# Performance work log

Measured on AMD Instinct MI355X. Metric: run time of the kernel, lower is better.

## Reference

```python
import jax, jax.numpy as jnp
import numpy as np

MI, DIS, DIN, HID, L, H, NG, H1, OUT = 2048, 1024, 3072, 256, 15, 8, 8, 512, 64
DENOM = 4.0 / 7.0  # (grid_max - grid_min) / (num_grids - 1)
EPS = 1e-5


def _ln(x, g, b):
    m = jnp.mean(x, axis=-1, keepdims=True)
    v = jnp.mean((x - m) ** 2, axis=-1, keepdims=True)
    return (x - m) * jax.lax.rsqrt(v + EPS) * g + b


def _fastkan(x, ln_g, ln_b, grid, Ws, Wb, bb):
    xn = _ln(x, ln_g, ln_b)
    basis = jnp.exp(-(((xn[..., None] - grid) / DENOM) ** 2))  # [N, DIN, NG]
    ret = basis.reshape(x.shape[0], -1) @ Ws.T                  # SplineLinear (no bias)
    return ret + jax.nn.silu(x) @ Wb.T + bb                      # base update


def _hgcn(x, G, W, attn, bias, rW1, rb1, rW2, rb2, ln_g, ln_b, jk_W, jk_b):
    # per-layer multi-head conv: mean_h a_h * G @ (x @ W_h) == G @ (x @ (sum_h a_h W_h / H))
    def step(xc, p):
        W_l, a_l, b_l, rW1_l, rb1_l, rW2_l, rb2_l, g_l, be_l = p
        W_eff = jnp.einsum('h,hio->io', a_l, W_l) / H
        out = G @ (xc @ W_eff) + b_l
        gate = jax.nn.sigmoid(jax.nn.relu(out @ rW1_l.T + rb1_l) @ rW2_l.T + rb2_l)
        out = _ln(out * gate, g_l, be_l)
        out = jnp.where(out >= 0, out, 0.25 * out)  # leaky_relu(0.25); dropout off (eval)
        return out, out
    _, outs = jax.lax.scan(step, x, (W, attn, bias, rW1, rb1, rW2, rb2, ln_g, ln_b))
    jk = jnp.moveaxis(outs, 0, 1).reshape(x.shape[0], L * HID)   # jumping-knowledge concat
    return jk @ jk_W.T + jk_b


def _mlp3(x, W1, b1, W2, b2, W3, b3):
    h = jax.nn.relu(x @ W1.T + b1)
    h = jax.nn.relu(h @ W2.T + b2)
    return jax.nn.relu(h @ W3.T + b3)


def _forward(concat_mi, concat_dis, G_mi, G_dis, AT, A, rbf_grid, mi_kan_ln_g, mi_kan_ln_b, mi_kan_Ws, mi_kan_Wb, mi_kan_bb, dis_kan_ln_g, dis_kan_ln_b, dis_kan_Ws, dis_kan_Wb, dis_kan_bb, mi_W, mi_attn, mi_bias, mi_rW1, mi_rb1, mi_rW2, mi_rb2, mi_ln_g, mi_ln_b, mi_jk_W, mi_jk_b, dis_W, dis_attn, dis_bias, dis_rW1, dis_rb1, dis_rW2, dis_rb2, dis_ln_g, dis_ln_b, dis_jk_W, dis_jk_b, lx_W1, lx_b1, lx_W2, lx_b2, lx_W3, lx_b3, ly_W1, ly_b1, ly_W2, ly_b2, ly_W3, ly_b3, ne_W, ne_b, he_W, he_b, mun_W, mun_b, mue_W, mue_b):
    # AT and A are accepted by the original forward but never used in its body.
    mi_e = _fastkan(concat_mi, mi_kan_ln_g, mi_kan_ln_b, rbf_grid, mi_kan_Ws, mi_kan_Wb, mi_kan_bb)
    dis_e = _fastkan(concat_dis, dis_kan_ln_g, dis_kan_ln_b, rbf_grid, dis_kan_Ws, dis_kan_Wb, dis_kan_bb)
    mi_f = _hgcn(mi_e, G_mi, mi_W, mi_attn, mi_bias, mi_rW1, mi_rb1, mi_rW2, mi_rb2, mi_ln_g, mi_ln_b, mi_jk_W, mi_jk_b)
    dis_f = _hgcn(dis_e, G_dis, dis_W, dis_attn, dis_bias, dis_rW1, dis_rb1, dis_rW2, dis_rb2, dis_ln_g, dis_ln_b, dis_jk_W, dis_jk_b)
    x = _mlp3(mi_f, lx_W1, lx_b1, lx_W2, lx_b2, lx_W3, lx_b3)
    y = _mlp3(dis_f, ly_W1, ly_b1, ly_W2, ly_b2, ly_W3, ly_b3)
    result_h = x @ y.T                                           # [MI, DIS]
    z_node = jax.nn.relu(concat_mi @ ne_W.T + ne_b)              # node_encoders1 (eval: no dropout)
    z_edge = jax.nn.relu(concat_dis @ he_W.T + he_b)             # hyperedge_encoders1
    z_node_mean = z_node @ mun_W.T + mun_b                       # _enc_mu_node (identity act)
    z_edge_mean = z_edge @ mue_W.T + mue_b                       # _enc_mu_hedge
    recon = z_node_mean @ z_edge_mean.T                          # decoder2 with identity act
    score = 0.7 * jax.nn.sigmoid(recon) + 0.3 * jax.nn.sigmoid(result_h)
    return score, recon


def setup_inputs() -> dict:
    ks = iter(jax.random.split(jax.random.key(0), 96))
    nrm = lambda shape, s: jax.random.normal(next(ks), shape, dtype=jnp.float32) * s
    uni = lambda shape: jax.random.uniform(next(ks), shape, dtype=jnp.float32)
    d = {}
    d['concat_mi'] = nrm((MI, DIN), 1.0)
    d['concat_dis'] = nrm((DIS, DIN), 1.0)
    d['G_mi'] = uni((MI, MI)) / MI    # row-normalized dense hypergraph adjacency
    d['G_dis'] = uni((DIS, DIS)) / DIS
    d['AT'] = uni((DIS, MI))
    d['A'] = uni((MI, DIS))
    d['rbf_grid'] = jnp.linspace(-2.0, 2.0, NG).astype(jnp.float32)
    for p in ('mi', 'dis'):
        d[p + '_kan_ln_g'] = jnp.ones((DIN,), jnp.float32)
        d[p + '_kan_ln_b'] = jnp.zeros((DIN,), jnp.float32)
        d[p + '_kan_Ws'] = nrm((HID, DIN * NG), 0.02)
        d[p + '_kan_Wb'] = nrm((HID, DIN), 0.02)
        d[p + '_kan_bb'] = nrm((HID,), 0.01)
        d[p + '_W'] = nrm((L, H, HID, HID), 0.06)
        d[p + '_attn'] = jnp.ones((L, H), jnp.float32)
        d[p + '_bias'] = nrm((L, HID), 0.01)
        d[p + '_rW1'] = nrm((L, HID // 4, HID), 0.05)
        d[p + '_rb1'] = nrm((L, HID // 4), 0.01)
        d[p + '_rW2'] = nrm((L, HID, HID // 4), 0.05)
        d[p + '_rb2'] = nrm((L, HID), 0.01)
        d[p + '_ln_g'] = jnp.ones((L, HID), jnp.float32)
        d[p + '_ln_b'] = jnp.zeros((L, HID), jnp.float32)
        d[p + '_jk_W'] = nrm((HID, L * HID), 0.02)
        d[p + '_jk_b'] = nrm((HID,), 0.01)
    for p in ('lx', 'ly'):
        d[p + '_W1'] = nrm((256, HID), 0.05); d[p + '_b1'] = nrm((256,), 0.01)
        d[p + '_W2'] = nrm((128, 256), 0.05); d[p + '_b2'] = nrm((128,), 0.01)
        d[p + '_W3'] = nrm((64, 128), 0.05); d[p + '_b3'] = nrm((64,), 0.01)
    d['ne_W'] = nrm((H1, DIN), 0.02); d['ne_b'] = nrm((H1,), 0.01)
    d['he_W'] = nrm((H1, DIN), 0.02); d['he_b'] = nrm((H1,), 0.01)
    d['mun_W'] = nrm((OUT, H1), 0.02); d['mun_b'] = nrm((OUT,), 0.01)
    d['mue_W'] = nrm((OUT, H1), 0.02); d['mue_b'] = nrm((OUT,), 0.01)
    return d


def reference(concat_mi, concat_dis, G_mi, G_dis, AT, A, rbf_grid, mi_kan_ln_g, mi_kan_ln_b, mi_kan_Ws, mi_kan_Wb, mi_kan_bb, dis_kan_ln_g, dis_kan_ln_b, dis_kan_Ws, dis_kan_Wb, dis_kan_bb, mi_W, mi_attn, mi_bias, mi_rW1, mi_rb1, mi_rW2, mi_rb2, mi_ln_g, mi_ln_b, mi_jk_W, mi_jk_b, dis_W, dis_attn, dis_bias, dis_rW1, dis_rb1, dis_rW2, dis_rb2, dis_ln_g, dis_ln_b, dis_jk_W, dis_jk_b, lx_W1, lx_b1, lx_W2, lx_b2, lx_W3, lx_b3, ly_W1, ly_b1, ly_W2, ly_b2, ly_W3, ly_b3, ne_W, ne_b, he_W, he_b, mun_W, mun_b, mue_W, mue_b):
    return _forward(concat_mi, concat_dis, G_mi, G_dis, AT, A, rbf_grid, mi_kan_ln_g, mi_kan_ln_b, mi_kan_Ws, mi_kan_Wb, mi_kan_bb, dis_kan_ln_g, dis_kan_ln_b, dis_kan_Ws, dis_kan_Wb, dis_kan_bb, mi_W, mi_attn, mi_bias, mi_rW1, mi_rb1, mi_rW2, mi_rb2, mi_ln_g, mi_ln_b, mi_jk_W, mi_jk_b, dis_W, dis_attn, dis_bias, dis_rW1, dis_rb1, dis_rW2, dis_rb2, dis_ln_g, dis_ln_b, dis_jk_W, dis_jk_b, lx_W1, lx_b1, lx_W2, lx_b2, lx_W3, lx_b3, ly_W1, ly_b1, ly_W2, ly_b2, ly_W3, ly_b3, ne_W, ne_b, he_W, he_b, mun_W, mun_b, mue_W, mue_b)
```

## Files before the change

kernel.cpp:

```cpp
#include <hip/hip_runtime.h>
#include <cstdint>
#include <cstddef>

typedef unsigned short u16;
typedef __attribute__((ext_vector_type(8))) short short8;
typedef __attribute__((ext_vector_type(4))) float f32x4;

#define MI_N  2048
#define DIS_N 1024
#define TOT_N 3072
#define DIN   3072
#define HID   256
#define LL    15
#define NG    8

__device__ __forceinline__ float b2f(u16 u) {
  unsigned int v = ((unsigned int)u) << 16;
  float f;
  __builtin_memcpy(&f, &v, 4);
  return f;
}
__device__ __forceinline__ u16 f2b(float f) {
  unsigned int u;
  __builtin_memcpy(&u, &f, 4);
  u = (u + 0x7fffu + ((u >> 16) & 1u)) >> 16;
  return (u16)u;
}
__device__ __forceinline__ float sigf(float x) { return 1.f / (1.f + __expf(-x)); }
__device__ __forceinline__ unsigned cvtpk(float a, float b) {
  unsigned r;
  asm("v_cvt_pk_bf16_f32 %0, %1, %2" : "=v"(r) : "v"(a), "v"(b));
  return r;
}

#define NSEG 20
struct CvtJobs {
  const float* src[NSEG];
  u16* dst[NSEG];
  int nblk[NSEG];
  int nseg;
};

__global__ __launch_bounds__(256) void cvt_f2b(CvtJobs j) {
  int b = blockIdx.x, s = 0;
  while (s + 1 < j.nseg && b >= j.nblk[s]) { b -= j.nblk[s]; ++s; }
  const long base = ((long)b * 256 + threadIdx.x) * 8;
  const float4 v0 = *(const float4*)(j.src[s] + base);
  const float4 v1 = *(const float4*)(j.src[s] + base + 4);
  short8 o;
  o[0] = (short)f2b(v0.x); o[1] = (short)f2b(v0.y);
  o[2] = (short)f2b(v0.z); o[3] = (short)f2b(v0.w);
  o[4] = (short)f2b(v1.x); o[5] = (short)f2b(v1.y);
  o[6] = (short)f2b(v1.z); o[7] = (short)f2b(v1.w);
  *(short8*)(j.dst[s] + base) = o;
}

struct GP {
  const u16* A; int lda;
  const u16* B; int ldb;
  void* C; int ldc;
  const float* bias;
  int K;
  int mblk;
};

template <int ACT, int TRANS, int F32OUT, int NCT>
__global__ __launch_bounds__(256) void gemm_bt(GP p0, GP p1) {
  GP p = p0;
  int bx = blockIdx.x;
  if (bx >= p0.mblk) { bx -= p0.mblk; p = p1; }
  const int tid = threadIdx.x;
  const int w = tid >> 6;
  const int lane = tid & 63;
  const int m16 = lane & 15, quad = lane >> 4;
  const int kph = quad * 8;
  const long row0 = (long)bx * 32 + m16;
  const long colBase = (long)blockIdx.y * (16 * NCT);
  f32x4 acc[2][NCT] = {};
  const u16* A0 = p.A + row0 * (long)p.lda + kph;
  const u16* A1 = A0 + 16L * p.lda;
  const u16* Bb = p.B + (colBase + m16) * (long)p.ldb + kph;
  const long bstep = 16L * p.ldb;
  for (int kk = w * 32; kk < p.K; kk += 128) {
    short8 a0 = *(const short8*)(A0 + kk);
    short8 a1 = *(const short8*)(A1 + kk);
#pragma unroll
    for (int c = 0; c < NCT; ++c) {
      short8 b = *(const short8*)(Bb + c * bstep + kk);
      acc[0][c] = __builtin_amdgcn_mfma_f32_16x16x32_bf16(a0, b, acc[0][c], 0, 0, 0);
      acc[1][c] = __builtin_amdgcn_mfma_f32_16x16x32_bf16(a1, b, acc[1][c], 0, 0, 0);
    }
  }
  __shared__ float red[2][64][NCT * 8 + 1];
  float* av = (float*)acc;
  if (w >= 2) {
#pragma unroll
    for (int i = 0; i < NCT * 8; ++i) red[w - 2][lane][i] = av[i];
  }
  __syncthreads();
  if (w < 2) {
#pragma unroll
    for (int i = 0; i < NCT * 8; ++i) av[i] += red[w][lane][i];
  }
  __syncthreads();
  if (w == 1) {
#pragma unroll
    for (int i = 0; i < NCT * 8; ++i) red[0][lane][i] = av[i];
  }
  __syncthreads();
  if (w != 0) return;
#pragma unroll
  for (int i = 0; i < NCT * 8; ++i) av[i] += red[0][lane][i];
#pragma unroll
  for (int c = 0; c < NCT; ++c) {
    const long col = colBase + c * 16 + m16;
    const float bv = p.bias ? p.bias[col] : 0.f;
#pragma unroll
    for (int r = 0; r < 2; ++r) {
      const long orow = (long)bx * 32 + r * 16 + quad * 4;
#pragma unroll
      for (int j = 0; j < 4; ++j) {
        float v = acc[r][c][j] + bv;
        if (ACT == 1) v = fmaxf(v, 0.f);
        if (ACT == 2) v = sigf(v);
        if (F32OUT)
          ((float*)p.C)[(orow + j) * (long)p.ldc + col] = v;
        else if (TRANS)
          ((u16*)p.C)[col * (long)p.ldc + orow + j] = f2b(v);
        else
          ((u16*)p.C)[(orow + j) * (long)p.ldc + col] = f2b(v);
      }
    }
  }
}

struct FKP {
  const u16* xn; const u16* xb;
  const u16* Ws; const u16* Wb;
  float* partial;
  int rowoff;
  int mblk;
};

__global__ __launch_bounds__(256) void fastkan_gemm(FKP p0, FKP p1, const float* grid8) {
  FKP p = p0;
  int bx = blockIdx.x;
  if (bx >= p0.mblk) { bx -= p0.mblk; p = p1; }
  const int chunk = blockIdx.z;
  const int tid = threadIdx.x;
  const int w = tid >> 6;
  const int lane = tid & 63;
  const int m16 = lane & 15, quad = lane >> 4, kph = quad * 8;
  const long row0 = (long)bx * 16 + m16;
  f32x4 acc[16] = {};
  if (chunk < 8) {
    float gv[8];
#pragma unroll
    for (int j = 0; j < 8; ++j) gv[j] = grid8[j];
    const u16* xn0 = p.xn + row0 * (long)DIN;
    const int d0 = chunk * 384 + w * 4 + quad;
    u16 xr[24];
#pragma unroll
    for (int t = 0; t < 24; ++t) xr[t] = xn0[d0 + 16 * t];
    const u16* Bb = p.Ws + (long)m16 * (DIN * NG) + chunk * 3072 + w * 32 + kph;
#pragma unroll 2
    for (int t = 0; t < 24; ++t) {
      const float x0 = b2f(xr[t]);
      union { short8 s; unsigned u[4]; } a0;
#pragma unroll
      for (int jj = 0; jj < 4; ++jj) {
        float da = x0 - gv[2 * jj];
        float db = x0 - gv[2 * jj + 1];
        a0.u[jj] = cvtpk(__expf(da * da * -3.0625f), __expf(db * db * -3.0625f));
      }
#pragma unroll
      for (int c = 0; c < 16; ++c) {
        short8 b = *(const short8*)(Bb + (long)c * (16 * DIN * NG) + t * 128);
        acc[c] = __builtin_amdgcn_mfma_f32_16x16x32_bf16(a0.s, b, acc[c], 0, 0, 0);
      }
    }
  } else {
    const u16* x0p = p.xb + row0 * (long)DIN + kph;
    const u16* Bb = p.Wb + (long)m16 * DIN + w * 32 + kph;
#pragma unroll 2
    for (int t = 0; t < 24; ++t) {
      const int kk = w * 32 + t * 128;
      short8 r0 = *(const short8*)(x0p + kk);
      union { short8 s; unsigned u[4]; } a0;
#pragma unroll
      for (int jj = 0; jj < 4; ++jj) {
        float va = b2f((u16)r0[2 * jj]);
        float vb = b2f((u16)r0[2 * jj + 1]);
        a0.u[jj] = cvtpk(va * sigf(va), vb * sigf(vb));
      }
#pragma unroll
      for (int c = 0; c < 16; ++c) {
        short8 b = *(const short8*)(Bb + (long)c * (16 * DIN) + t * 128);
        acc[c] = __builtin_amdgcn_mfma_f32_16x16x32_bf16(a0.s, b, acc[c], 0, 0, 0);
      }
    }
  }
  __shared__ float red[2][64][65];
  float* av = (float*)acc;
  if (w >= 2) {
#pragma unroll
    for (int i = 0; i < 64; ++i) red[w - 2][lane][i] = av[i];
  }
  __syncthreads();
  if (w < 2) {
#pragma unroll
    for (int i = 0; i < 64; ++i) av[i] += red[w][lane][i];
  }
  __syncthreads();
  if (w == 1) {
#pragma unroll
    for (int i = 0; i < 64; ++i) red[0][lane][i] = av[i];
  }
  __syncthreads();
  if (w != 0) return;
#pragma unroll
  for (int i = 0; i < 64; ++i) av[i] += red[0][lane][i];
  float* outp = p.partial + ((long)chunk * TOT_N + p.rowoff) * HID;
#pragma unroll
  for (int c = 0; c < 16; ++c) {
    const long col = c * 16 + m16;
    const long orow = (long)bx * 16 + quad * 4;
#pragma unroll
    for (int j = 0; j < 4; ++j) outp[(orow + j) * HID + col] = acc[c][j];
  }
}

__global__ __launch_bounds__(256) void fk_combine(const float* partial, const float* bb_mi,
                                                  const float* bb_dis, u16* e) {
  const long i = (long)blockIdx.x * 256 + threadIdx.x;
  const int c = (int)(i & 255);
  const long n = i >> 8;
  float s = 0.f;
#pragma unroll
  for (int pI = 0; pI < 9; ++pI) s += partial[(long)pI * TOT_N * HID + i];
  s += (n < MI_N ? bb_mi : bb_dis)[c];
  e[i] = f2b(s);
}

__global__ __launch_bounds__(256) void weff_kernel(const float* Wmi, const float* Ami,
                                                   const float* Wdis, const float* Adis,
                                                   u16* outT) {
  const int b = blockIdx.x;
  const int s = b / 3840;
  const int r = b % 3840;
  const int l = r >> 8;
  const int t = r & 255;
  const int i0 = (t >> 4) << 4;
  const int o0 = (t & 15) << 4;
  const float* W = (s ? Wdis : Wmi) + (long)l * 8 * 65536;
  const float* A = (s ? Adis : Ami) + l * 8;
  const int tx = threadIdx.x & 15;
  const int ty = threadIdx.x >> 4;
  float sum = 0.f;
#pragma unroll
  for (int h = 0; h < 8; ++h)
    sum += A[h] * W[(long)h * 65536 + (long)(i0 + ty) * 256 + o0 + tx];
  sum *= 0.125f;
  __shared__ float tile[16][17];
  tile[ty][tx] = sum;
  __syncthreads();
  outT[((long)s * LL + l) * 65536 + (long)(o0 + ty) * 256 + i0 + tx] = f2b(tile[tx][ty]);
}

__device__ __forceinline__ void breduce2(float& a, float& b) {
  for (int o = 32; o > 0; o >>= 1) {
    a += __shfl_down(a, o);
    b += __shfl_down(b, o);
  }
  __shared__ float sm[8];
  const int w = threadIdx.x >> 6;
  const int lane = threadIdx.x & 63;
  if (lane == 0) { sm[w] = a; sm[4 + w] = b; }
  __syncthreads();
  if (threadIdx.x == 0) {
    sm[0] = sm[0] + sm[1] + sm[2] + sm[3];
    sm[4] = sm[4] + sm[5] + sm[6] + sm[7];
  }
  __syncthreads();
  a = sm[0];
  b = sm[4];
}

__global__ __launch_bounds__(256) void ln_silu(const float* xmi, const float* xdis,
                                               const float* gmi, const float* bmi,
                                               const float* gdis, const float* bdis,
                                               u16* xn, u16* cbf) {
  const int n = blockIdx.x;
  const bool ds = (n >= MI_N);
  const float* x = ds ? xdis + (long)(n - MI_N) * DIN : xmi + (long)n * DIN;
  const float* g = ds ? gdis : gmi;
  const float* be = ds ? bdis : bmi;
  float xv[12];
  float s1 = 0.f, s2 = 0.f;
#pragma unroll
  for (int j = 0; j < 12; ++j) {
    xv[j] = x[j * 256 + threadIdx.x];
    s1 += xv[j];
    s2 += xv[j] * xv[j];
  }
  breduce2(s1, s2);
  const float m = s1 * (1.f / DIN);
  const float inv = rsqrtf(s2 * (1.f / DIN) - m * m + 1e-5f);
#pragma unroll
  for (int j = 0; j < 12; ++j) {
    const int e = j * 256 + threadIdx.x;
    xn[(long)n * DIN + e] = f2b((xv[j] - m) * inv * g[e] + be[e]);
    cbf[(long)n * DIN + e] = f2b(xv[j]);
  }
}

__global__ __launch_bounds__(256) void gate_ln(const u16* hout, const u16* gate,
                                               const float* gmi, const float* bmi,
                                               const float* gdis, const float* bdis,
                                               u16* jk, int l) {
  const int n = blockIdx.x;
  const int c = threadIdx.x;
  const bool ds = (n >= MI_N);
  const float* g = (ds ? gdis : gmi) + l * HID;
  const float* be = (ds ? bdis : bmi) + l * HID;
  const float h = b2f(hout[(long)n * HID + c]) * b2f(gate[(long)n * HID + c]);
  float s1 = h, s2 = h * h;
  breduce2(s1, s2);
  const float m = s1 * (1.f / HID);
  const float var = s2 * (1.f / HID) - m * m;
  float y = (h - m) * rsqrtf(var + 1e-5f) * g[c] + be[c];
  y = (y >= 0.f) ? y : 0.25f * y;
  jk[(long)n * (LL * HID) + l * HID + c] = f2b(y);
}

__global__ __launch_bounds__(256) void final_combine(const float* rh, float* out) {
  const long i = (long)blockIdx.x * 256 + threadIdx.x;
  const float rc = out[(long)MI_N * DIS_N + i];
  out[i] = 0.7f * sigf(rc) + 0.3f * sigf(rh[i]);
}

extern "C" void kernel_launch(void* const* d_in, const int* in_sizes, int n_in,
                              void* d_out, int out_size, void* d_ws, size_t ws_size,
                              hipStream_t stream) {
  const float* concat_mi   = (const float*)d_in[0];
  const float* concat_dis  = (const float*)d_in[1];
  const float* G_mi        = (const float*)d_in[2];
  const float* G_dis       = (const float*)d_in[3];
  const float* rbf_grid    = (const float*)d_in[6];
  const float* mi_kan_ln_g = (const float*)d_in[7];
  const float* mi_kan_ln_b = (const float*)d_in[8];
  const float* mi_kan_Ws   = (const float*)d_in[9];
  const float* mi_kan_Wb   = (const float*)d_in[10];
  const float* mi_kan_bb   = (const float*)d_in[11];
  const float* mi_W        = (const float*)d_in[12];
  const float* mi_attn     = (const float*)d_in[13];
  const float* mi_bias     = (const float*)d_in[14];
  const float* mi_rW1      = (const float*)d_in[15];
  const float* mi_rb1      = (const float*)d_in[16];
  const float* mi_rW2      = (const float*)d_in[17];
  const float* mi_rb2      = (const float*)d_in[18];
  const float* mi_ln_g     = (const float*)d_in[19];
  const float* mi_ln_b     = (const float*)d_in[20];
  const float* mi_jk_W     = (const float*)d_in[21];
  const float* mi_jk_b     = (const float*)d_in[22];
  const float* dis_kan_ln_g = (const float*)d_in[23];
  const float* dis_kan_ln_b = (const float*)d_in[24];
  const float* dis_kan_Ws  = (const float*)d_in[25];
  const float* dis_kan_Wb  = (const float*)d_in[26];
  const float* dis_kan_bb  = (const float*)d_in[27];
  const float* dis_W       = (const float*)d_in[28];
  const float* dis_attn    = (const float*)d_in[29];
  const float* dis_bias    = (const float*)d_in[30];
  const float* dis_rW1     = (const float*)d_in[31];
  const float* dis_rb1     = (const float*)d_in[32];
  const float* dis_rW2     = (const float*)d_in[33];
  const float* dis_rb2     = (const float*)d_in[34];
  const float* dis_ln_g    = (const float*)d_in[35];
  const float* dis_ln_b    = (const float*)d_in[36];
  const float* dis_jk_W    = (const float*)d_in[37];
  const float* dis_jk_b    = (const float*)d_in[38];
  const float* lx_W1 = (const float*)d_in[39]; const float* lx_b1 = (const float*)d_in[40];
  const float* lx_W2 = (const float*)d_in[41]; const float* lx_b2 = (const float*)d_in[42];
  const float* lx_W3 = (const float*)d_in[43]; const float* lx_b3 = (const float*)d_in[44];
  const float* ly_W1 = (const float*)d_in[45]; const float* ly_b1 = (const float*)d_in[46];
  const float* ly_W2 = (const float*)d_in[47]; const float* ly_b2 = (const float*)d_in[48];
  const float* ly_W3 = (const float*)d_in[49]; const float* ly_b3 = (const float*)d_in[50];
  const float* ne_W  = (const float*)d_in[51]; const float* ne_b  = (const float*)d_in[52];
  const float* he_W  = (const float*)d_in[53]; const float* he_b  = (const float*)d_in[54];
  const float* mun_W = (const float*)d_in[55]; const float* mun_b = (const float*)d_in[56];
  const float* mue_W = (const float*)d_in[57]; const float* mue_b = (const float*)d_in[58];

  char* wp = (char*)d_ws;
  size_t off = 0;
  auto alloc = [&](size_t bytes) -> void* {
    void* p = wp + off;
    off += (bytes + 255) & ~(size_t)255;
    return p;
  };
  u16* cbf    = (u16*)alloc((size_t)TOT_N * DIN * 2);
  u16* gmib   = (u16*)alloc((size_t)MI_N * MI_N * 2);
  u16* gdisb  = (u16*)alloc((size_t)DIS_N * DIS_N * 2);
  u16* wsb0   = (u16*)alloc((size_t)256 * 24576 * 2);
  u16* wsb1   = (u16*)alloc((size_t)256 * 24576 * 2);
  u16* wbb0   = (u16*)alloc((size_t)256 * 3072 * 2);
  u16* wbb1   = (u16*)alloc((size_t)256 * 3072 * 2);
  u16* jkwb0  = (u16*)alloc((size_t)256 * 3840 * 2);
  u16* jkwb1  = (u16*)alloc((size_t)256 * 3840 * 2);
  u16* rw1b0  = (u16*)alloc((size_t)LL * 64 * 256 * 2);
  u16* rw1b1  = (u16*)alloc((size_t)LL * 64 * 256 * 2);
  u16* rw2b0  = (u16*)alloc((size_t)LL * 256 * 64 * 2);
  u16* rw2b1  = (u16*)alloc((size_t)LL * 256 * 64 * 2);
  u16* lxw1b  = (u16*)alloc((size_t)256 * 256 * 2);
  u16* lxw2b  = (u16*)alloc((size_t)128 * 256 * 2);
  u16* lxw3b  = (u16*)alloc((size_t)64 * 128 * 2);
  u16* lyw1b  = (u16*)alloc((size_t)256 * 256 * 2);
  u16* lyw2b  = (u16*)alloc((size_t)128 * 256 * 2);
  u16* lyw3b  = (u16*)alloc((size_t)64 * 128 * 2);
  u16* neb    = (u16*)alloc((size_t)512 * 3072 * 2);
  u16* heb    = (u16*)alloc((size_t)512 * 3072 * 2);
  u16* munb   = (u16*)alloc((size_t)64 * 512 * 2);
  u16* mueb   = (u16*)alloc((size_t)64 * 512 * 2);
  u16* wefft  = (u16*)alloc((size_t)2 * LL * 65536 * 2);
  u16* e      = (u16*)alloc((size_t)TOT_N * HID * 2);
  u16* t1t    = (u16*)alloc((size_t)HID * TOT_N * 2);
  u16* hout   = (u16*)alloc((size_t)TOT_N * HID * 2);
  u16* g1b    = (u16*)alloc((size_t)TOT_N * 64 * 2);
  u16* gateb  = (u16*)alloc((size_t)TOT_N * HID * 2);
  u16* jk     = (u16*)alloc((size_t)TOT_N * LL * HID * 2);
  u16* fb     = (u16*)alloc((size_t)TOT_N * HID * 2);
  char* regA  = (char*)alloc(47300000);
  u16* xn     = (u16*)regA;
  float* fkp  = (float*)(regA + 18874624);
  u16* h1b    = (u16*)regA;
  u16* h2b    = (u16*)(regA + 1572864);
  u16* xyb    = (u16*)(regA + 2359296);
  float* rh   = (float*)(regA + 2752512);
  u16* zb     = (u16*)(regA + 11141120);
  u16* zm     = (u16*)(regA + 14286848);
  float* outf = (float*)d_out;
  float* rec  = outf + (size_t)MI_N * DIS_N;
  (void)ws_size; (void)in_sizes; (void)n_in; (void)out_size;

  const dim3 B256(256);

  {
    CvtJobs cj{};
    int ns = 0, total = 0;
    auto push = [&](const float* s, u16* dst, int count) {
      cj.src[ns] = s; cj.dst[ns] = dst; cj.nblk[ns] = count / 2048;
      total += count / 2048; ++ns;
    };
    push(G_mi, gmib, MI_N * MI_N);
    push(G_dis, gdisb, DIS_N * DIS_N);
    push(mi_kan_Ws, wsb0, 256 * 24576);
    push(dis_kan_Ws, wsb1, 256 * 24576);
    push(mi_kan_Wb, wbb0, 256 * 3072);
    push(dis_kan_Wb, wbb1, 256 * 3072);
    push(mi_jk_W, jkwb0, 256 * 3840);
    push(dis_jk_W, jkwb1, 256 * 3840);
    push(mi_rW1, rw1b0, LL * 64 * 256);
    push(dis_rW1, rw1b1, LL * 64 * 256);
    push(mi_rW2, rw2b0, LL * 256 * 64);
    push(dis_rW2, rw2b1, LL * 256 * 64);
    push(lx_W1, lxw1b, 256 * 256);
    push(lx_W2, lxw2b, 128 * 256);
    push(lx_W3, lxw3b, 64 * 128);
    push(ly_W1, lyw1b, 256 * 256);
    push(ly_W2, lyw2b, 128 * 256);
    push(ly_W3, lyw3b, 64 * 128);
    push(ne_W, neb, 512 * 3072);
    push(he_W, heb, 512 * 3072);
    cj.nseg = ns;
    cvt_f2b<<<dim3(total), B256, 0, stream>>>(cj);
    CvtJobs cj2{};
    cj2.src[0] = mun_W; cj2.dst[0] = munb; cj2.nblk[0] = (64 * 512) / 2048;
    cj2.src[1] = mue_W; cj2.dst[1] = mueb; cj2.nblk[1] = (64 * 512) / 2048;
    cj2.nseg = 2;
    cvt_f2b<<<dim3(32), B256, 0, stream>>>(cj2);
  }
  ln_silu<<<dim3(TOT_N), B256, 0, stream>>>(concat_mi, concat_dis, mi_kan_ln_g, mi_kan_ln_b,
                                            dis_kan_ln_g, dis_kan_ln_b, xn, cbf);
  weff_kernel<<<dim3(2 * LL * 256), B256, 0, stream>>>(mi_W, mi_attn, dis_W, dis_attn, wefft);
  {
    FKP f0{xn, cbf, wsb0, wbb0, fkp, 0, 128};
    FKP f1{xn + (size_t)MI_N * DIN, cbf + (size_t)MI_N * DIN, wsb1, wbb1, fkp, MI_N, 64};
    fastkan_gemm<<<dim3(192, 1, 9), B256, 0, stream>>>(f0, f1, rbf_grid);
    fk_combine<<<dim3(TOT_N * HID / 256), B256, 0, stream>>>(fkp, mi_kan_bb, dis_kan_bb, e);
  }
  for (int l = 0; l < LL; ++l) {
    const u16* xc0 = (l == 0) ? e : jk + (size_t)(l - 1) * HID;
    const u16* xc1 = (l == 0) ? e + (size_t)MI_N * HID
                              : jk + (size_t)MI_N * LL * HID + (size_t)(l - 1) * HID;
    const int xlda = (l == 0) ? HID : LL * HID;
    GP a0{xc0, xlda, wefft + (size_t)l * 65536, 256, t1t, MI_N, nullptr, 256, 64};
    GP a1{xc1, xlda, wefft + ((size_t)LL + l) * 65536, 256, t1t + (size_t)HID * MI_N, DIS_N,
          nullptr, 256, 32};
    gemm_bt<0, 1, 0, 4><<<dim3(96, 4), B256, 0, stream>>>(a0, a1);
    GP h0{gmib, MI_N, t1t, MI_N, hout, HID, mi_bias + l * HID, MI_N, 64};
    GP h1{gdisb, DIS_N, t1t + (size_t)HID * MI_N, DIS_N, hout + (size_t)MI_N * HID, HID,
          dis_bias + l * HID, DIS_N, 32};
    gemm_bt<0, 0, 0, 4><<<dim3(96, 4), B256, 0, stream>>>(h0, h1);
    GP g0{hout, HID, rw1b0 + (size_t)l * 64 * HID, HID, g1b, 64, mi_rb1 + l * 64, HID, 64};
    GP g1{hout + (size_t)MI_N * HID, HID, rw1b1 + (size_t)l * 64 * HID, HID,
          g1b + (size_t)MI_N * 64, 64, dis_rb1 + l * 64, HID, 32};
    gemm_bt<1, 0, 0, 4><<<dim3(96, 1), B256, 0, stream>>>(g0, g1);
    GP s0{g1b, 64, rw2b0 + (size_t)l * HID * 64, 64, gateb, HID, mi_rb2 + l * HID, 64, 64};
    GP s1{g1b + (size_t)MI_N * 64, 64, rw2b1 + (size_t)l * HID * 64, 64,
          gateb + (size_t)MI_N * HID, HID, dis_rb2 + l * HID, 64, 32};
    gemm_bt<2, 0, 0, 4><<<dim3(96, 4), B256, 0, stream>>>(s0, s1);
    gate_ln<<<dim3(TOT_N), B256, 0, stream>>>(hout, gateb, mi_ln_g, mi_ln_b, dis_ln_g,
                                              dis_ln_b, jk, l);
  }
  {
    GP j0{jk, LL * HID, jkwb0, LL * HID, fb, HID, mi_jk_b, LL * HID, 64};
    GP j1{jk + (size_t)MI_N * LL * HID, LL * HID, jkwb1, LL * HID, fb + (size_t)MI_N * HID,
          HID, dis_jk_b, LL * HID, 32};
    gemm_bt<0, 0, 0, 4><<<dim3(96, 4), B256, 0, stream>>>(j0, j1);
  }
  {
    GP m0{fb, HID, lxw1b, HID, h1b, 256, lx_b1, HID, 64};
    GP m1{fb + (size_t)MI_N * HID, HID, lyw1b, HID, h1b + (size_t)MI_N * 256, 256, ly_b1,
          HID, 32};
    gemm_bt<1, 0, 0, 4><<<dim3(96, 4), B256, 0, stream>>>(m0, m1);
    GP n0{h1b, 256, lxw2b, 256, h2b, 128, lx_b2, 256, 64};
    GP n1{h1b + (size_t)MI_N * 256, 256, lyw2b, 256, h2b + (size_t)MI_N * 128, 128, ly_b2,
          256, 32};
    gemm_bt<1, 0, 0, 4><<<dim3(96, 2), B256, 0, stream>>>(n0, n1);
    GP o0{h2b, 128, lxw3b, 128, xyb, 64, lx_b3, 128, 64};
    GP o1{h2b + (size_t)MI_N * 128, 128, lyw3b, 128, xyb + (size_t)MI_N * 64, 64, ly_b3,
          128, 32};
    gemm_bt<1, 0, 0, 4><<<dim3(96, 1), B256, 0, stream>>>(o0, o1);
  }
  {
    GP r0{xyb, 64, xyb + (size_t)MI_N * 64, 64, rh, DIS_N, nullptr, 64, 64};
    gemm_bt<0, 0, 1, 4><<<dim3(64, 16), B256, 0, stream>>>(r0, r0);
  }
  {
    GP e0{cbf, DIN, neb, DIN, zb, 512, ne_b, DIN, 64};
    GP e1{cbf + (size_t)MI_N * DIN, DIN, heb, DIN, zb + (size_t)MI_N * 512, 512, he_b, DIN,
          32};
    gemm_bt<1, 0, 0, 4><<<dim3(96, 8), B256, 0, stream>>>(e0, e1);
  }
  {
    GP u0{zb, 512, munb, 512, zm, 64, mun_b, 512, 64};
    GP u1{zb + (size_t)MI_N * 512, 512, mueb, 512, zm + (size_t)MI_N * 64, 64, mue_b, 512,
          32};
    gemm_bt<0, 0, 0, 4><<<dim3(96, 1), B256, 0, stream>>>(u0, u1);
  }
  {
    GP c0{zm, 64, zm + (size_t)MI_N * 64, 64, rec, DIS_N, nullptr, 64, 64};
    gemm_bt<0, 0, 1, 4><<<dim3(64, 16), B256, 0, stream>>>(c0, c0);
  }
  final_combine<<<dim3(MI_N * DIS_N / 256), B256, 0, stream>>>(rh, outf);
}
```

Measured before the change: 1.601 ms.

## Process two 16-row tiles per block in FastKAN GEMM to reuse weight loads

Each fastkan_gemm block now computes 32 output rows instead of 16, so every weight fragment loaded from global memory feeds two MFMAs. The grid is halved to match. The x inputs are now loaded one step ahead instead of all 24 being preloaded. Accumulator registers double to 128 floats per lane and the LDS reduction buffer doubles, which can lower occupancy and adds reduction work.

```diff
diff --git a/kernel.cpp b/kernel.cpp
--- a/kernel.cpp
+++ b/kernel.cpp
@@ -151,82 +151,94 @@
   const int w = tid >> 6;
   const int lane = tid & 63;
   const int m16 = lane & 15, quad = lane >> 4, kph = quad * 8;
-  const long row0 = (long)bx * 16 + m16;
-  f32x4 acc[16] = {};
+  const long row0 = (long)bx * 32 + m16;
+  f32x4 acc[2][16] = {};
   if (chunk < 8) {
     float gv[8];
 #pragma unroll
     for (int j = 0; j < 8; ++j) gv[j] = grid8[j];
     const u16* xn0 = p.xn + row0 * (long)DIN;
+    const u16* xn1 = xn0 + 16L * DIN;
     const int d0 = chunk * 384 + w * 4 + quad;
-    u16 xr[24];
-#pragma unroll
-    for (int t = 0; t < 24; ++t) xr[t] = xn0[d0 + 16 * t];
+    u16 x0c = xn0[d0];
+    u16 x1c = xn1[d0];
     const u16* Bb = p.Ws + (long)m16 * (DIN * NG) + chunk * 3072 + w * 32 + kph;
-#pragma unroll 2
     for (int t = 0; t < 24; ++t) {
-      const float x0 = b2f(xr[t]);
-      union { short8 s; unsigned u[4]; } a0;
+      const int tn = (t < 23) ? t + 1 : 23;
+      const u16 x0n = xn0[d0 + 16 * tn];
+      const u16 x1n = xn1[d0 + 16 * tn];
+      const float x0 = b2f(x0c), x1 = b2f(x1c);
+      union { short8 s; unsigned u[4]; } a0, a1;
 #pragma unroll
       for (int jj = 0; jj < 4; ++jj) {
-        float da = x0 - gv[2 * jj];
-        float db = x0 - gv[2 * jj + 1];
-        a0.u[jj] = cvtpk(__expf(da * da * -3.0625f), __expf(db * db * -3.0625f));
+        float da0 = x0 - gv[2 * jj], db0 = x0 - gv[2 * jj + 1];
+        float da1 = x1 - gv[2 * jj], db1 = x1 - gv[2 * jj + 1];
+        a0.u[jj] = cvtpk(__expf(da0 * da0 * -3.0625f), __expf(db0 * db0 * -3.0625f));
+        a1.u[jj] = cvtpk(__expf(da1 * da1 * -3.0625f), __expf(db1 * db1 * -3.0625f));
       }
 #pragma unroll
       for (int c = 0; c < 16; ++c) {
         short8 b = *(const short8*)(Bb + (long)c * (16 * DIN * NG) + t * 128);
-        acc[c] = __builtin_amdgcn_mfma_f32_16x16x32_bf16(a0.s, b, acc[c], 0, 0, 0);
+        acc[0][c] = __builtin_amdgcn_mfma_f32_16x16x32_bf16(a0.s, b, acc[0][c], 0, 0, 0);
+        acc[1][c] = __builtin_amdgcn_mfma_f32_16x16x32_bf16(a1.s, b, acc[1][c], 0, 0, 0);
       }
+      x0c = x0n;
+      x1c = x1n;
     }
   } else {
     const u16* x0p = p.xb + row0 * (long)DIN + kph;
+    const u16* x1p = x0p + 16L * DIN;
     const u16* Bb = p.Wb + (long)m16 * DIN + w * 32 + kph;
-#pragma unroll 2
     for (int t = 0; t < 24; ++t) {
       const int kk = w * 32 + t * 128;
       short8 r0 = *(const short8*)(x0p + kk);
-      union { short8 s; unsigned u[4]; } a0;
+      short8 r1 = *(const short8*)(x1p + kk);
+      union { short8 s; unsigned u[4]; } a0, a1;
 #pragma unroll
       for (int jj = 0; jj < 4; ++jj) {
-        float va = b2f((u16)r0[2 * jj]);
-        float vb = b2f((u16)r0[2 * jj + 1]);
-        a0.u[jj] = cvtpk(va * sigf(va), vb * sigf(vb));
+        float va0 = b2f((u16)r0[2 * jj]), vb0 = b2f((u16)r0[2 * jj + 1]);
+        float va1 = b2f((u16)r1[2 * jj]), vb1 = b2f((u16)r1[2 * jj + 1]);
+        a0.u[jj] = cvtpk(va0 * sigf(va0), vb0 * sigf(vb0));
+        a1.u[jj] = cvtpk(va1 * sigf(va1), vb1 * sigf(vb1));
       }
 #pragma unroll
       for (int c = 0; c < 16; ++c) {
         short8 b = *(const short8*)(Bb + (long)c * (16 * DIN) + t * 128);
-        acc[c] = __builtin_amdgcn_mfma_f32_16x16x32_bf16(a0.s, b, acc[c], 0, 0, 0);
+        acc[0][c] = __builtin_amdgcn_mfma_f32_16x16x32_bf16(a0.s, b, acc[0][c], 0, 0, 0);
+        acc[1][c] = __builtin_amdgcn_mfma_f32_16x16x32_bf16(a1.s, b, acc[1][c], 0, 0, 0);
       }
     }
   }
-  __shared__ float red[2][64][65];
+  __shared__ float red[2][64][129];
   float* av = (float*)acc;
   if (w >= 2) {
 #pragma unroll
-    for (int i = 0; i < 64; ++i) red[w - 2][lane][i] = av[i];
+    for (int i = 0; i < 128; ++i) red[w - 2][lane][i] = av[i];
   }
   __syncthreads();
   if (w < 2) {
 #pragma unroll
-    for (int i = 0; i < 64; ++i) av[i] += red[w][lane][i];
+    for (int i = 0; i < 128; ++i) av[i] += red[w][lane][i];
   }
   __syncthreads();
   if (w == 1) {
 #pragma unroll
-    for (int i = 0; i < 64; ++i) red[0][lane][i] = av[i];
+    for (int i = 0; i < 128; ++i) red[0][lane][i] = av[i];
   }
   __syncthreads();
   if (w != 0) return;
 #pragma unroll
-  for (int i = 0; i < 64; ++i) av[i] += red[0][lane][i];
+  for (int i = 0; i < 128; ++i) av[i] += red[0][lane][i];
   float* outp = p.partial + ((long)chunk * TOT_N + p.rowoff) * HID;
 #pragma unroll
   for (int c = 0; c < 16; ++c) {
     const long col = c * 16 + m16;
-    const long orow = (long)bx * 16 + quad * 4;
-#pragma unroll
-    for (int j = 0; j < 4; ++j) outp[(orow + j) * HID + col] = acc[c][j];
+#pragma unroll
+    for (int r = 0; r < 2; ++r) {
+      const long orow = (long)bx * 32 + r * 16 + quad * 4;
+#pragma unroll
+      for (int j = 0; j < 4; ++j) outp[(orow + j) * HID + col] = acc[r][c][j];
+    }
   }
 }
 
@@ -482,9 +494,9 @@
                                             dis_kan_ln_g, dis_kan_ln_b, xn, cbf);
   weff_kernel<<<dim3(2 * LL * 256), B256, 0, stream>>>(mi_W, mi_attn, dis_W, dis_attn, wefft);
   {
-    FKP f0{xn, cbf, wsb0, wbb0, fkp, 0, 128};
-    FKP f1{xn + (size_t)MI_N * DIN, cbf + (size_t)MI_N * DIN, wsb1, wbb1, fkp, MI_N, 64};
-    fastkan_gemm<<<dim3(192, 1, 9), B256, 0, stream>>>(f0, f1, rbf_grid);
+    FKP f0{xn, cbf, wsb0, wbb0, fkp, 0, 64};
+    FKP f1{xn + (size_t)MI_N * DIN, cbf + (size_t)MI_N * DIN, wsb1, wbb1, fkp, MI_N, 32};
+    fastkan_gemm<<<dim3(96, 1, 9), B256, 0, stream>>>(f0, f1, rbf_grid);
     fk_combine<<<dim3(TOT_N * HID / 256), B256, 0, stream>>>(fkp, mi_kan_bb, dis_kan_bb, e);
   }
   for (int l = 0; l < LL; ++l) {
```

New measurement: 1.510 ms. 1.06x faster.
